# Optimization experiments

Hardware: AMD Instinct MI355X
Metric: run time of the kernel (lower is better)

Reference implementation:

```python
import jax, jax.numpy as jnp
import numpy as np

NUM_EXPERTS = 8
HIDDEN_DIM = 2048
EXPERT_DIM = 1408
TOP_K = 2
NUM_TOKENS = 8192


def setup_inputs() -> dict:
    key = jax.random.key(0)
    k_x, k_idx, k_s, k_up, k_dn = jax.random.split(key, 5)
    x = jax.random.normal(k_x, (NUM_TOKENS, HIDDEN_DIM), dtype=jnp.float32)
    expert_indices = jax.random.randint(k_idx, (NUM_TOKENS, TOP_K), 0, NUM_EXPERTS, dtype=jnp.int64)
    scores = jax.random.uniform(k_s, (NUM_TOKENS, TOP_K), dtype=jnp.float32)
    up_proj = jax.random.normal(k_up, (NUM_EXPERTS, HIDDEN_DIM, 2 * EXPERT_DIM), dtype=jnp.float32) * 0.02
    down_proj = jax.random.normal(k_dn, (NUM_EXPERTS, EXPERT_DIM, HIDDEN_DIM), dtype=jnp.float32) * 0.02
    return {"x": x, "expert_indices": expert_indices, "scores": scores,
            "up_proj": up_proj, "down_proj": down_proj}


def reference(x, expert_indices, scores, up_proj, down_proj):
    # x: [T, H]; expert_indices/scores: [T, K]; up_proj: [E, H, 2D]; down_proj: [E, D, H]
    E = up_proj.shape[0]
    D = down_proj.shape[1]
    out = jnp.zeros_like(x)
    # Loop over small fixed set of experts; each token's output is the score-weighted
    # sum over the experts it was routed to (SwiGLU gated FFN per expert).
    for e in range(E):
        # combined routing weight of expert e for each token: [T]
        w_e = jnp.sum(scores * (expert_indices == e).astype(scores.dtype), axis=-1)
        h = x @ up_proj[e]                      # [T, 2D]
        gate, up = h[:, :D], h[:, D:]
        y = (jax.nn.silu(gate) * up) @ down_proj[e]  # [T, H]
        out = out + w_e[:, None] * y
    return out
```

## Files before the change

### kernel.cpp

```cpp
#include <hip/hip_runtime.h>
#include <hip/hip_bf16.h>
#include <cstdint>
#include <cstddef>

#define N_EXPERTS 8
#define HIDDEN    2048
#define EDIM      1408
#define UPCOLS    2816
#define NTOK      8192
#define CAP       8192
#define MAXMT     136
#define NS_UP     22
#define NS_DN     16
#define GUP       6
#define GDN       8

typedef __bf16 bf16x8 __attribute__((ext_vector_type(8)));
typedef __bf16 bf16x4 __attribute__((ext_vector_type(4)));
typedef float  f32x4  __attribute__((ext_vector_type(4)));

#define EPOS_OFF  4096
#define TOK_OFF   (EPOS_OFF + (size_t)NTOK * 2 * 4)
#define W_OFF     (TOK_OFF + (size_t)CAP * N_EXPERTS * 4)
#define XBF_OFF   (W_OFF + (size_t)CAP * N_EXPERTS * 4)
#define UPT_OFF   (XBF_OFF + (size_t)NTOK * HIDDEN * 2)
#define DNT_OFF   (UPT_OFF + (size_t)N_EXPERTS * UPCOLS * HIDDEN * 2)
#define HACT_OFF  (DNT_OFF + (size_t)N_EXPERTS * HIDDEN * EDIM * 2)
#define WS_NEEDED (HACT_OFF + (size_t)(MAXMT * 128) * EDIM * 2)
#define YBUF_OFF  UPT_OFF


__device__ __forceinline__ void gload16(const void* g, void* l) {
  __builtin_amdgcn_global_load_lds(
      (const __attribute__((address_space(1))) void*)g,
      (__attribute__((address_space(3))) void*)l, 16, 0, 0);
}

__global__ void build_entries(const int* __restrict__ idx,
                              const float* __restrict__ sc,
                              int* __restrict__ meta,
                              int* __restrict__ toks,
                              float* __restrict__ wts,
                              int* __restrict__ epos) {
  int t = blockIdx.x * blockDim.x + threadIdx.x;
  if (t >= NTOK) return;
  int e0 = idx[2 * t] & 7, e1 = idx[2 * t + 1] & 7;
  float s0 = sc[2 * t], s1 = sc[2 * t + 1];
  if (e0 == e1) {
    int p = atomicAdd(&meta[e0], 1);
    toks[e0 * CAP + p] = t; wts[e0 * CAP + p] = s0 + s1;
    epos[2 * t] = (e0 << 16) | p; epos[2 * t + 1] = -1;
  } else {
    int p0 = atomicAdd(&meta[e0], 1);
    toks[e0 * CAP + p0] = t; wts[e0 * CAP + p0] = s0;
    int p1 = atomicAdd(&meta[e1], 1);
    toks[e1 * CAP + p1] = t; wts[e1 * CAP + p1] = s1;
    epos[2 * t] = (e0 << 16) | p0; epos[2 * t + 1] = (e1 << 16) | p1;
  }
}

__global__ void finalize_meta(int* __restrict__ meta,
                              int* __restrict__ toks,
                              float* __restrict__ wts) {
  __shared__ int c[8], pc[8];
  int tid = threadIdx.x;
  if (tid < 8) { c[tid] = meta[tid]; pc[tid] = ((c[tid] + 127) >> 7) << 7; }
  __syncthreads();
  if (tid == 0) {
    int off = 0, t = 0;
    for (int e = 0; e < 8; e++) {
      meta[16 + e] = off;
      int nt = pc[e] >> 7;
      for (int i = 0; i < nt; i++) { meta[32 + t] = e; meta[192 + t] = i * 128; t++; }
      off += pc[e];
    }
    meta[8] = t;
  }
  for (int e = 0; e < 8; e++)
    for (int i = c[e] + tid; i < pc[e]; i += blockDim.x) {
      toks[e * CAP + i] = 0; wts[e * CAP + i] = 0.f;
    }
}

__global__ void cast_x(const float4* __restrict__ in, __bf16* __restrict__ o) {
  size_t i = (size_t)blockIdx.x * blockDim.x + threadIdx.x;
  float4 v = in[i];
  bf16x4 r = { (__bf16)v.x, (__bf16)v.y, (__bf16)v.z, (__bf16)v.w };
  ((bf16x4*)o)[i] = r;
}

__global__ void transpose_cast(const float* __restrict__ in, __bf16* __restrict__ out,
                               int K, int N) {
  __shared__ float t[32][33];
  const size_t ebase = (size_t)blockIdx.z * K * N;
  const float* src = in + ebase;
  __bf16* dst = out + ebase;
  int x0 = blockIdx.x * 32, y0 = blockIdx.y * 32;
  int tx = threadIdx.x, ty = threadIdx.y;
#pragma unroll
  for (int i = 0; i < 4; i++)
    t[ty + 8 * i][tx] = src[(size_t)(y0 + ty + 8 * i) * N + x0 + tx];
  __syncthreads();
#pragma unroll
  for (int i = 0; i < 4; i++)
    dst[(size_t)(x0 + ty + 8 * i) * K + y0 + tx] = (__bf16)t[tx][ty + 8 * i];
}


__global__ __launch_bounds__(256, 4) void gemm_up(
    const __bf16* __restrict__ xb, const __bf16* __restrict__ upT,
    const int* __restrict__ meta, const int* __restrict__ toks,
    __bf16* __restrict__ hact) {
  const int rank = (blockIdx.x & 7) * (MAXMT * NS_UP / 8) + (blockIdx.x >> 3);
  const int vt = rank / NS_UP;
  if (vt >= meta[8]) return;
  const int e = meta[32 + vt];
  const int tb = vt - (meta[192 + vt] >> 7);
  const int tiles_e = (meta[e] + 127) >> 7;
  int rem = rank - NS_UP * tb;
  int g = 0, tleft = tiles_e;
  for (;;) {
    int gsz = tleft < GUP ? tleft : GUP;
    int span = NS_UP * gsz;
    if (rem < span) break;
    rem -= span; tleft -= GUP; g++;
  }
  const int gsz = tleft < GUP ? tleft : GUP;
  const int s = rem / gsz, tix = rem - s * gsz;
  const int row0 = (g * GUP + tix) * 128;
  const int hbase = meta[16 + e];
  const int n0 = s * 64;

  __shared__ __bf16 lA[128 * 64];
  __shared__ __bf16 lBg[64 * 64];
  __shared__ __bf16 lBu[64 * 64];

  const int tid = threadIdx.x;
  const int lane = tid & 63, wave = tid >> 6;
  const int srow = tid >> 3;
  const int gch = (tid & 7) ^ (srow & 7);

  const __bf16* upE = upT + (size_t)e * UPCOLS * HIDDEN;

  size_t aoff[4];
#pragma unroll
  for (int r = 0; r < 4; r++) {
    int row = row0 + srow + 32 * r;
    int tok = toks[e * CAP + row];
    aoff[r] = (size_t)tok * HIDDEN + gch * 8;
  }
  size_t bgoff[2], buoff[2];
#pragma unroll
  for (int r = 0; r < 2; r++) {
    int n = n0 + srow + 32 * r;
    bgoff[r] = (size_t)n * HIDDEN + gch * 8;
    buoff[r] = (size_t)(n + EDIM) * HIDDEN + gch * 8;
  }

  f32x4 accg[4][2] = {};
  f32x4 accu[4][2] = {};
  const int wrow = (wave >> 1) * 64;
  const int wcol = (wave & 1) * 32;
  const int l15 = lane & 15, quad = lane >> 4;

  for (int k0 = 0; k0 < HIDDEN; k0 += 64) {
    __syncthreads();
#pragma unroll
    for (int r = 0; r < 4; r++)
      gload16(xb + aoff[r] + k0, (char*)lA + r * 4096 + tid * 16);
#pragma unroll
    for (int r = 0; r < 2; r++) {
      gload16(upE + bgoff[r] + k0, (char*)lBg + r * 4096 + tid * 16);
      gload16(upE + buoff[r] + k0, (char*)lBu + r * 4096 + tid * 16);
    }
    __syncthreads();
#pragma unroll
    for (int kk = 0; kk < 2; kk++) {
      bf16x8 af[4], bg[2], bu[2];
#pragma unroll
      for (int mi = 0; mi < 4; mi++) {
        int row = wrow + mi * 16 + l15;
        int slot = (kk * 4 + quad) ^ (row & 7);
        af[mi] = *(const bf16x8*)((const char*)lA + row * 128 + slot * 16);
      }
#pragma unroll
      for (int ni = 0; ni < 2; ni++) {
        int row = wcol + ni * 16 + l15;
        int slot = (kk * 4 + quad) ^ (row & 7);
        bg[ni] = *(const bf16x8*)((const char*)lBg + row * 128 + slot * 16);
        bu[ni] = *(const bf16x8*)((const char*)lBu + row * 128 + slot * 16);
      }
#pragma unroll
      for (int mi = 0; mi < 4; mi++)
#pragma unroll
        for (int ni = 0; ni < 2; ni++) {
          accg[mi][ni] = __builtin_amdgcn_mfma_f32_16x16x32_bf16(af[mi], bg[ni], accg[mi][ni], 0, 0, 0);
          accu[mi][ni] = __builtin_amdgcn_mfma_f32_16x16x32_bf16(af[mi], bu[ni], accu[mi][ni], 0, 0, 0);
        }
    }
  }

#pragma unroll
  for (int mi = 0; mi < 4; mi++)
#pragma unroll
    for (int ni = 0; ni < 2; ni++)
#pragma unroll
      for (int v = 0; v < 4; v++) {
        int m = hbase + row0 + wrow + mi * 16 + quad * 4 + v;
        int n = n0 + wcol + ni * 16 + l15;
        float g = accg[mi][ni][v];
        float u = accu[mi][ni][v];
        float act = g / (1.f + __expf(-g)) * u;
        hact[(size_t)m * EDIM + n] = (__bf16)act;
      }
}

__global__ __launch_bounds__(256, 4) void gemm_down(
    const __bf16* __restrict__ hact, const __bf16* __restrict__ dnT,
    const int* __restrict__ meta, const float* __restrict__ wts,
    __bf16* __restrict__ ybuf) {
  const int rank = (blockIdx.x & 7) * (MAXMT * NS_DN / 8) + (blockIdx.x >> 3);
  const int vt = rank / NS_DN;
  if (vt >= meta[8]) return;
  const int e = meta[32 + vt];
  const int tb = vt - (meta[192 + vt] >> 7);
  const int tiles_e = (meta[e] + 127) >> 7;
  int rem = rank - NS_DN * tb;
  int g = 0, tleft = tiles_e;
  for (;;) {
    int gsz = tleft < GDN ? tleft : GDN;
    int span = NS_DN * gsz;
    if (rem < span) break;
    rem -= span; tleft -= GDN; g++;
  }
  const int gsz = tleft < GDN ? tleft : GDN;
  const int s = rem / gsz, tix = rem - s * gsz;
  const int row0 = (g * GDN + tix) * 128;
  const int hbase = meta[16 + e];
  const int n0 = s * 128;

  __shared__ __bf16 lA[128 * 64];
  __shared__ __bf16 lB[128 * 64];

  const int tid = threadIdx.x;
  const int lane = tid & 63, wave = tid >> 6;
  const int srow = tid >> 3;
  const int gch = (tid & 7) ^ (srow & 7);

  const __bf16* dnE = dnT + (size_t)e * HIDDEN * EDIM;

  size_t aoff[4], boff[4];
#pragma unroll
  for (int r = 0; r < 4; r++) {
    int row = srow + 32 * r;
    aoff[r] = (size_t)(hbase + row0 + row) * EDIM + gch * 8;
    boff[r] = (size_t)(n0 + row) * EDIM + gch * 8;
  }

  f32x4 acc[4][4] = {};
  const int wrow = (wave >> 1) * 64;
  const int wcol = (wave & 1) * 64;
  const int l15 = lane & 15, quad = lane >> 4;

  for (int k0 = 0; k0 < EDIM; k0 += 64) {
    __syncthreads();
#pragma unroll
    for (int r = 0; r < 4; r++) {
      gload16(hact + aoff[r] + k0, (char*)lA + r * 4096 + tid * 16);
      gload16(dnE + boff[r] + k0, (char*)lB + r * 4096 + tid * 16);
    }
    __syncthreads();
#pragma unroll
    for (int kk = 0; kk < 2; kk++) {
      bf16x8 af[4], bfr[4];
#pragma unroll
      for (int mi = 0; mi < 4; mi++) {
        int row = wrow + mi * 16 + l15;
        int slot = (kk * 4 + quad) ^ (row & 7);
        af[mi] = *(const bf16x8*)((const char*)lA + row * 128 + slot * 16);
      }
#pragma unroll
      for (int ni = 0; ni < 4; ni++) {
        int row = wcol + ni * 16 + l15;
        int slot = (kk * 4 + quad) ^ (row & 7);
        bfr[ni] = *(const bf16x8*)((const char*)lB + row * 128 + slot * 16);
      }
#pragma unroll
      for (int mi = 0; mi < 4; mi++)
#pragma unroll
        for (int ni = 0; ni < 4; ni++)
          acc[mi][ni] = __builtin_amdgcn_mfma_f32_16x16x32_bf16(af[mi], bfr[ni], acc[mi][ni], 0, 0, 0);
    }
  }

#pragma unroll
  for (int mi = 0; mi < 4; mi++)
#pragma unroll
    for (int v = 0; v < 4; v++) {
      int rloc = row0 + wrow + mi * 16 + quad * 4 + v;
      float w = wts[e * CAP + rloc];
      size_t g2 = (size_t)(hbase + rloc) * HIDDEN;
#pragma unroll
      for (int ni = 0; ni < 4; ni++) {
        int n = n0 + wcol + ni * 16 + l15;
        ybuf[g2 + n] = (__bf16)(acc[mi][ni][v] * w);
      }
    }
}

__global__ __launch_bounds__(256) void combine(
    const __bf16* __restrict__ ybuf, const int* __restrict__ epos,
    const int* __restrict__ meta, float* __restrict__ out) {
  const int t = blockIdx.x;
  const int c = threadIdx.x * 8;
  const int p0 = epos[2 * t], p1 = epos[2 * t + 1];
  const int e0 = p0 >> 16;
  const size_t g0 = (size_t)(meta[16 + e0] + (p0 & 0xffff)) * HIDDEN;
  bf16x8 y0 = *(const bf16x8*)(ybuf + g0 + c);
  float acc[8];
#pragma unroll
  for (int j = 0; j < 8; j++) acc[j] = (float)y0[j];
  if (p1 >= 0) {
    const int e1 = p1 >> 16;
    const size_t g1 = (size_t)(meta[16 + e1] + (p1 & 0xffff)) * HIDDEN;
    bf16x8 y1 = *(const bf16x8*)(ybuf + g1 + c);
#pragma unroll
    for (int j = 0; j < 8; j++) acc[j] += (float)y1[j];
  }
  float4* o = (float4*)(out + (size_t)t * HIDDEN + c);
  o[0] = make_float4(acc[0], acc[1], acc[2], acc[3]);
  o[1] = make_float4(acc[4], acc[5], acc[6], acc[7]);
}

extern "C" void kernel_launch(void* const* d_in, const int* in_sizes, int n_in,
                              void* d_out, int out_size, void* d_ws, size_t ws_size,
                              hipStream_t stream) {
  const float* x = (const float*)d_in[0];
  const int* idx = (const int*)d_in[1];
  const float* sc = (const float*)d_in[2];
  const float* up = (const float*)d_in[3];
  const float* dn = (const float*)d_in[4];
  float* out = (float*)d_out;
  char* ws = (char*)d_ws;

  if (ws_size < WS_NEEDED) return;

  int* meta = (int*)ws;
  int* epos = (int*)(ws + EPOS_OFF);
  int* toks = (int*)(ws + TOK_OFF);
  float* wts = (float*)(ws + W_OFF);
  __bf16* xb = (__bf16*)(ws + XBF_OFF);
  __bf16* upT = (__bf16*)(ws + UPT_OFF);
  __bf16* dnT = (__bf16*)(ws + DNT_OFF);
  __bf16* hact = (__bf16*)(ws + HACT_OFF);
  __bf16* ybuf = (__bf16*)(ws + YBUF_OFF);

  hipMemsetAsync(meta, 0, 64, stream);

  build_entries<<<NTOK / 256, 256, 0, stream>>>(idx, sc, meta, toks, wts, epos);
  finalize_meta<<<1, 256, 0, stream>>>(meta, toks, wts);
  cast_x<<<(NTOK * HIDDEN / 4) / 256, 256, 0, stream>>>((const float4*)x, xb);
  dim3 tb(32, 8);
  transpose_cast<<<dim3(UPCOLS / 32, HIDDEN / 32, N_EXPERTS), tb, 0, stream>>>(up, upT, HIDDEN, UPCOLS);
  transpose_cast<<<dim3(HIDDEN / 32, EDIM / 32, N_EXPERTS), tb, 0, stream>>>(dn, dnT, EDIM, HIDDEN);
  gemm_up<<<MAXMT * NS_UP, 256, 0, stream>>>(xb, upT, meta, toks, hact);
  gemm_down<<<MAXMT * NS_DN, 256, 0, stream>>>(hact, dnT, meta, wts, ybuf);
  combine<<<NTOK, 256, 0, stream>>>(ybuf, epos, meta, out);
}
```

Baseline: 766.3 us.

## Use 256x256 tiles with double-buffered LDS pipeline in expert GEMMs

Both expert GEMMs move from 128-row tiles on 256 threads to 256-row by 256-column tiles on 512 threads (8 waves), padding expert capacity to multiples of 256. LDS is double-buffered so the next K slice is loaded asynchronously while MFMAs run on the current one, and the MFMA sections use explicit barriers and setprio. The aim is more data reuse per tile, fewer global loads per flop, and hiding load latency. In exchange, padding waste grows, fewer blocks are launched with 128KB of LDS each, and one-block-per-CU occupancy risks idle CUs on a few tail tiles.

New measurement: 936.7 us. 1.22x slower.

```diff
diff --git a/kernel.cpp b/kernel.cpp
--- a/kernel.cpp
+++ b/kernel.cpp
@@ -9,11 +9,13 @@
 #define UPCOLS    2816
 #define NTOK      8192
 #define CAP       8192
-#define MAXMT     136
-#define NS_UP     22
-#define NS_DN     16
-#define GUP       6
-#define GDN       8
+#define MAXT      72
+#define NS_UP     11
+#define NS_DN     8
+#define GUP       3
+#define GDN       4
+#define NT_UP     32
+#define NT_DN     22
 
 typedef __bf16 bf16x8 __attribute__((ext_vector_type(8)));
 typedef __bf16 bf16x4 __attribute__((ext_vector_type(4)));
@@ -26,7 +28,8 @@
 #define UPT_OFF   (XBF_OFF + (size_t)NTOK * HIDDEN * 2)
 #define DNT_OFF   (UPT_OFF + (size_t)N_EXPERTS * UPCOLS * HIDDEN * 2)
 #define HACT_OFF  (DNT_OFF + (size_t)N_EXPERTS * HIDDEN * EDIM * 2)
-#define WS_NEEDED (HACT_OFF + (size_t)(MAXMT * 128) * EDIM * 2)
+#define HACT_ROWS ((size_t)MAXT * 256)
+#define WS_NEEDED (HACT_OFF + HACT_ROWS * EDIM * 2)
 #define YBUF_OFF  UPT_OFF
 
 
@@ -64,14 +67,14 @@
                               float* __restrict__ wts) {
   __shared__ int c[8], pc[8];
   int tid = threadIdx.x;
-  if (tid < 8) { c[tid] = meta[tid]; pc[tid] = ((c[tid] + 127) >> 7) << 7; }
+  if (tid < 8) { c[tid] = meta[tid]; pc[tid] = ((c[tid] + 255) >> 8) << 8; }
   __syncthreads();
   if (tid == 0) {
     int off = 0, t = 0;
     for (int e = 0; e < 8; e++) {
       meta[16 + e] = off;
-      int nt = pc[e] >> 7;
-      for (int i = 0; i < nt; i++) { meta[32 + t] = e; meta[192 + t] = i * 128; t++; }
+      int nt = pc[e] >> 8;
+      for (int i = 0; i < nt; i++) { meta[32 + t] = e; meta[192 + t] = i * 256; t++; }
       off += pc[e];
     }
     meta[8] = t;
@@ -107,16 +110,16 @@
 }
 
 
-__global__ __launch_bounds__(256, 4) void gemm_up(
+__global__ __launch_bounds__(512, 2) void gemm_up(
     const __bf16* __restrict__ xb, const __bf16* __restrict__ upT,
     const int* __restrict__ meta, const int* __restrict__ toks,
     __bf16* __restrict__ hact) {
-  const int rank = (blockIdx.x & 7) * (MAXMT * NS_UP / 8) + (blockIdx.x >> 3);
+  const int rank = (blockIdx.x & 7) * (MAXT * NS_UP / 8) + (blockIdx.x >> 3);
   const int vt = rank / NS_UP;
   if (vt >= meta[8]) return;
   const int e = meta[32 + vt];
-  const int tb = vt - (meta[192 + vt] >> 7);
-  const int tiles_e = (meta[e] + 127) >> 7;
+  const int tb = vt - (meta[192 + vt] >> 8);
+  const int tiles_e = (meta[e] + 255) >> 8;
   int rem = rank - NS_UP * tb;
   int g = 0, tleft = tiles_e;
   for (;;) {
@@ -127,104 +130,128 @@
   }
   const int gsz = tleft < GUP ? tleft : GUP;
   const int s = rem / gsz, tix = rem - s * gsz;
-  const int row0 = (g * GUP + tix) * 128;
+  const int row0 = (g * GUP + tix) * 256;
   const int hbase = meta[16 + e];
-  const int n0 = s * 64;
-
-  __shared__ __bf16 lA[128 * 64];
-  __shared__ __bf16 lBg[64 * 64];
-  __shared__ __bf16 lBu[64 * 64];
+  const int n0 = s * 128;
+
+  __shared__ __attribute__((aligned(16))) char lds[131072];
 
   const int tid = threadIdx.x;
   const int lane = tid & 63, wave = tid >> 6;
+  const int wm = wave >> 2, wn = wave & 3;
+  const int l15 = lane & 15, quad = lane >> 4;
   const int srow = tid >> 3;
   const int gch = (tid & 7) ^ (srow & 7);
 
   const __bf16* upE = upT + (size_t)e * UPCOLS * HIDDEN;
 
-  size_t aoff[4];
+  size_t aoff[4], boff[4];
 #pragma unroll
   for (int r = 0; r < 4; r++) {
-    int row = row0 + srow + 32 * r;
+    int row = row0 + r * 64 + srow;
     int tok = toks[e * CAP + row];
     aoff[r] = (size_t)tok * HIDDEN + gch * 8;
   }
-  size_t bgoff[2], buoff[2];
-#pragma unroll
-  for (int r = 0; r < 2; r++) {
-    int n = n0 + srow + 32 * r;
-    bgoff[r] = (size_t)n * HIDDEN + gch * 8;
-    buoff[r] = (size_t)(n + EDIM) * HIDDEN + gch * 8;
-  }
-
-  f32x4 accg[4][2] = {};
-  f32x4 accu[4][2] = {};
-  const int wrow = (wave >> 1) * 64;
-  const int wcol = (wave & 1) * 32;
-  const int l15 = lane & 15, quad = lane >> 4;
-
-  for (int k0 = 0; k0 < HIDDEN; k0 += 64) {
-    __syncthreads();
-#pragma unroll
-    for (int r = 0; r < 4; r++)
-      gload16(xb + aoff[r] + k0, (char*)lA + r * 4096 + tid * 16);
-#pragma unroll
-    for (int r = 0; r < 2; r++) {
-      gload16(upE + bgoff[r] + k0, (char*)lBg + r * 4096 + tid * 16);
-      gload16(upE + buoff[r] + k0, (char*)lBu + r * 4096 + tid * 16);
+#pragma unroll
+  for (int j = 0; j < 4; j++) {
+    int grow = (srow < 32) ? (n0 + 32 * j + srow)
+                           : (EDIM + n0 + 32 * j + (srow - 32));
+    boff[j] = (size_t)grow * HIDDEN + gch * 8;
+  }
+
+  f32x4 acc[2][2][4][2] = {};
+
+  const int sl0 = (quad ^ (l15 & 7)) * 16;
+  const int sl1 = ((4 + quad) ^ (l15 & 7)) * 16;
+  const int aRowBase = wm * 16384 + l15 * 128;
+  const int bRowBase = 65536 + (wn >> 1) * 16384 + ((wn & 1) * 64 + l15) * 128;
+
+#define STAGE_UP(buf, k0) do {                                          \
+    char* _a = lds + (buf) * 32768;                                     \
+    char* _bb = lds + 65536 + (buf) * 32768;                            \
+    _Pragma("unroll")                                                   \
+    for (int r = 0; r < 4; r++)                                         \
+      gload16(xb + aoff[r] + (k0), _a + r * 8192 + tid * 16);           \
+    _Pragma("unroll")                                                   \
+    for (int r = 0; r < 4; r++)                                         \
+      gload16(upE + boff[r] + (k0), _bb + r * 8192 + tid * 16);         \
+  } while (0)
+
+#define PHASE_UP(cbuf, rh, ch) do {                                     \
+    const char* _l = lds + (cbuf) * 32768;                              \
+    bf16x8 a0[4], a1[4], b0[2], b1[2];                                  \
+    _Pragma("unroll")                                                   \
+    for (int mi = 0; mi < 4; mi++) {                                    \
+      int rb = aRowBase + (rh) * 8192 + mi * 2048;                      \
+      a0[mi] = *(const bf16x8*)(_l + rb + sl0);                         \
+      a1[mi] = *(const bf16x8*)(_l + rb + sl1);                         \
+    }                                                                   \
+    _Pragma("unroll")                                                   \
+    for (int ni = 0; ni < 2; ni++) {                                    \
+      int rb = bRowBase + (ch) * 4096 + ni * 2048;                      \
+      b0[ni] = *(const bf16x8*)(_l + rb + sl0);                         \
+      b1[ni] = *(const bf16x8*)(_l + rb + sl1);                         \
+    }                                                                   \
+    __builtin_amdgcn_s_barrier();                                       \
+    __builtin_amdgcn_s_setprio(1);                                      \
+    _Pragma("unroll")                                                   \
+    for (int mi = 0; mi < 4; mi++)                                      \
+      _Pragma("unroll")                                                 \
+      for (int ni = 0; ni < 2; ni++) {                                  \
+        acc[rh][ch][mi][ni] = __builtin_amdgcn_mfma_f32_16x16x32_bf16(  \
+            a0[mi], b0[ni], acc[rh][ch][mi][ni], 0, 0, 0);              \
+        acc[rh][ch][mi][ni] = __builtin_amdgcn_mfma_f32_16x16x32_bf16(  \
+            a1[mi], b1[ni], acc[rh][ch][mi][ni], 0, 0, 0);              \
+      }                                                                 \
+    __builtin_amdgcn_s_setprio(0);                                      \
+    __builtin_amdgcn_s_barrier();                                       \
+  } while (0)
+
+  STAGE_UP(0, 0);
+#pragma unroll 1
+  for (int kt = 0; kt < NT_UP; ++kt) {
+    const int c = kt & 1;
+    if (kt + 1 < NT_UP) {
+      STAGE_UP(c ^ 1, (kt + 1) * 64);
+      asm volatile("s_waitcnt vmcnt(8)" ::: "memory");
+    } else {
+      asm volatile("s_waitcnt vmcnt(0)" ::: "memory");
     }
-    __syncthreads();
-#pragma unroll
-    for (int kk = 0; kk < 2; kk++) {
-      bf16x8 af[4], bg[2], bu[2];
-#pragma unroll
-      for (int mi = 0; mi < 4; mi++) {
-        int row = wrow + mi * 16 + l15;
-        int slot = (kk * 4 + quad) ^ (row & 7);
-        af[mi] = *(const bf16x8*)((const char*)lA + row * 128 + slot * 16);
+    __builtin_amdgcn_s_barrier();
+    PHASE_UP(c, 0, 0); PHASE_UP(c, 0, 1);
+    PHASE_UP(c, 1, 0); PHASE_UP(c, 1, 1);
+  }
+#undef STAGE_UP
+#undef PHASE_UP
+
+#pragma unroll
+  for (int rh = 0; rh < 2; rh++)
+#pragma unroll
+    for (int mi = 0; mi < 4; mi++)
+#pragma unroll
+      for (int v = 0; v < 4; v++) {
+        int m = hbase + row0 + wm * 128 + rh * 64 + mi * 16 + quad * 4 + v;
+#pragma unroll
+        for (int ni = 0; ni < 2; ni++) {
+          int n = n0 + wn * 32 + ni * 16 + l15;
+          float gg = acc[rh][0][mi][ni][v];
+          float uu = acc[rh][1][mi][ni][v];
+          float act = gg / (1.f + __expf(-gg)) * uu;
+          hact[(size_t)m * EDIM + n] = (__bf16)act;
+        }
       }
-#pragma unroll
-      for (int ni = 0; ni < 2; ni++) {
-        int row = wcol + ni * 16 + l15;
-        int slot = (kk * 4 + quad) ^ (row & 7);
-        bg[ni] = *(const bf16x8*)((const char*)lBg + row * 128 + slot * 16);
-        bu[ni] = *(const bf16x8*)((const char*)lBu + row * 128 + slot * 16);
-      }
-#pragma unroll
-      for (int mi = 0; mi < 4; mi++)
-#pragma unroll
-        for (int ni = 0; ni < 2; ni++) {
-          accg[mi][ni] = __builtin_amdgcn_mfma_f32_16x16x32_bf16(af[mi], bg[ni], accg[mi][ni], 0, 0, 0);
-          accu[mi][ni] = __builtin_amdgcn_mfma_f32_16x16x32_bf16(af[mi], bu[ni], accu[mi][ni], 0, 0, 0);
-        }
-    }
-  }
-
-#pragma unroll
-  for (int mi = 0; mi < 4; mi++)
-#pragma unroll
-    for (int ni = 0; ni < 2; ni++)
-#pragma unroll
-      for (int v = 0; v < 4; v++) {
-        int m = hbase + row0 + wrow + mi * 16 + quad * 4 + v;
-        int n = n0 + wcol + ni * 16 + l15;
-        float g = accg[mi][ni][v];
-        float u = accu[mi][ni][v];
-        float act = g / (1.f + __expf(-g)) * u;
-        hact[(size_t)m * EDIM + n] = (__bf16)act;
-      }
-}
-
-__global__ __launch_bounds__(256, 4) void gemm_down(
+}
+
+__global__ __launch_bounds__(512, 2) void gemm_down(
     const __bf16* __restrict__ hact, const __bf16* __restrict__ dnT,
     const int* __restrict__ meta, const float* __restrict__ wts,
     __bf16* __restrict__ ybuf) {
-  const int rank = (blockIdx.x & 7) * (MAXMT * NS_DN / 8) + (blockIdx.x >> 3);
+  const int rank = (blockIdx.x & 7) * (MAXT * NS_DN / 8) + (blockIdx.x >> 3);
   const int vt = rank / NS_DN;
   if (vt >= meta[8]) return;
   const int e = meta[32 + vt];
-  const int tb = vt - (meta[192 + vt] >> 7);
-  const int tiles_e = (meta[e] + 127) >> 7;
+  const int tb = vt - (meta[192 + vt] >> 8);
+  const int tiles_e = (meta[e] + 255) >> 8;
   int rem = rank - NS_DN * tb;
   int g = 0, tleft = tiles_e;
   for (;;) {
@@ -235,15 +262,16 @@
   }
   const int gsz = tleft < GDN ? tleft : GDN;
   const int s = rem / gsz, tix = rem - s * gsz;
-  const int row0 = (g * GDN + tix) * 128;
+  const int row0 = (g * GDN + tix) * 256;
   const int hbase = meta[16 + e];
-  const int n0 = s * 128;
-
-  __shared__ __bf16 lA[128 * 64];
-  __shared__ __bf16 lB[128 * 64];
+  const int n0 = s * 256;
+
+  __shared__ __attribute__((aligned(16))) char lds[131072];
 
   const int tid = threadIdx.x;
   const int lane = tid & 63, wave = tid >> 6;
+  const int wm = wave >> 2, wn = wave & 3;
+  const int l15 = lane & 15, quad = lane >> 4;
   const int srow = tid >> 3;
   const int gch = (tid & 7) ^ (srow & 7);
 
@@ -252,60 +280,93 @@
   size_t aoff[4], boff[4];
 #pragma unroll
   for (int r = 0; r < 4; r++) {
-    int row = srow + 32 * r;
-    aoff[r] = (size_t)(hbase + row0 + row) * EDIM + gch * 8;
-    boff[r] = (size_t)(n0 + row) * EDIM + gch * 8;
-  }
-
-  f32x4 acc[4][4] = {};
-  const int wrow = (wave >> 1) * 64;
-  const int wcol = (wave & 1) * 64;
-  const int l15 = lane & 15, quad = lane >> 4;
-
-  for (int k0 = 0; k0 < EDIM; k0 += 64) {
-    __syncthreads();
-#pragma unroll
-    for (int r = 0; r < 4; r++) {
-      gload16(hact + aoff[r] + k0, (char*)lA + r * 4096 + tid * 16);
-      gload16(dnE + boff[r] + k0, (char*)lB + r * 4096 + tid * 16);
+    aoff[r] = (size_t)(hbase + row0 + r * 64 + srow) * EDIM + gch * 8;
+    boff[r] = (size_t)(n0 + r * 64 + srow) * EDIM + gch * 8;
+  }
+
+  f32x4 acc[2][2][4][2] = {};
+
+  const int sl0 = (quad ^ (l15 & 7)) * 16;
+  const int sl1 = ((4 + quad) ^ (l15 & 7)) * 16;
+  const int aRowBase = wm * 16384 + l15 * 128;
+  const int bRowBase = 65536 + (wn >> 1) * 16384 + ((wn & 1) * 64 + l15) * 128;
+
+#define STAGE_DN(buf, k0) do {                                          \
+    char* _a = lds + (buf) * 32768;                                     \
+    char* _bb = lds + 65536 + (buf) * 32768;                            \
+    _Pragma("unroll")                                                   \
+    for (int r = 0; r < 4; r++)                                         \
+      gload16(hact + aoff[r] + (k0), _a + r * 8192 + tid * 16);         \
+    _Pragma("unroll")                                                   \
+    for (int r = 0; r < 4; r++)                                         \
+      gload16(dnE + boff[r] + (k0), _bb + r * 8192 + tid * 16);         \
+  } while (0)
+
+#define PHASE_DN(cbuf, rh, ch) do {                                     \
+    const char* _l = lds + (cbuf) * 32768;                              \
+    bf16x8 a0[4], a1[4], b0[2], b1[2];                                  \
+    _Pragma("unroll")                                                   \
+    for (int mi = 0; mi < 4; mi++) {                                    \
+      int rb = aRowBase + (rh) * 8192 + mi * 2048;                      \
+      a0[mi] = *(const bf16x8*)(_l + rb + sl0);                         \
+      a1[mi] = *(const bf16x8*)(_l + rb + sl1);                         \
+    }                                                                   \
+    _Pragma("unroll")                                                   \
+    for (int ni = 0; ni < 2; ni++) {                                    \
+      int rb = bRowBase + (ch) * 4096 + ni * 2048;                      \
+      b0[ni] = *(const bf16x8*)(_l + rb + sl0);                         \
+      b1[ni] = *(const bf16x8*)(_l + rb + sl1);                         \
+    }                                                                   \
+    __builtin_amdgcn_s_barrier();                                       \
+    __builtin_amdgcn_s_setprio(1);                                      \
+    _Pragma("unroll")                                                   \
+    for (int mi = 0; mi < 4; mi++)                                      \
+      _Pragma("unroll")                                                 \
+      for (int ni = 0; ni < 2; ni++) {                                  \
+        acc[rh][ch][mi][ni] = __builtin_amdgcn_mfma_f32_16x16x32_bf16(  \
+            a0[mi], b0[ni], acc[rh][ch][mi][ni], 0, 0, 0);              \
+        acc[rh][ch][mi][ni] = __builtin_amdgcn_mfma_f32_16x16x32_bf16(  \
+            a1[mi], b1[ni], acc[rh][ch][mi][ni], 0, 0, 0);              \
+      }                                                                 \
+    __builtin_amdgcn_s_setprio(0);                                      \
+    __builtin_amdgcn_s_barrier();                                       \
+  } while (0)
+
+  STAGE_DN(0, 0);
+#pragma unroll 1
+  for (int kt = 0; kt < NT_DN; ++kt) {
+    const int c = kt & 1;
+    if (kt + 1 < NT_DN) {
+      STAGE_DN(c ^ 1, (kt + 1) * 64);
+      asm volatile("s_waitcnt vmcnt(8)" ::: "memory");
+    } else {
+      asm volatile("s_waitcnt vmcnt(0)" ::: "memory");
     }
-    __syncthreads();
-#pragma unroll
-    for (int kk = 0; kk < 2; kk++) {
-      bf16x8 af[4], bfr[4];
-#pragma unroll
-      for (int mi = 0; mi < 4; mi++) {
-        int row = wrow + mi * 16 + l15;
-        int slot = (kk * 4 + quad) ^ (row & 7);
-        af[mi] = *(const bf16x8*)((const char*)lA + row * 128 + slot * 16);
+    __builtin_amdgcn_s_barrier();
+    PHASE_DN(c, 0, 0); PHASE_DN(c, 0, 1);
+    PHASE_DN(c, 1, 0); PHASE_DN(c, 1, 1);
+  }
+#undef STAGE_DN
+#undef PHASE_DN
+
+#pragma unroll
+  for (int rh = 0; rh < 2; rh++)
+#pragma unroll
+    for (int mi = 0; mi < 4; mi++)
+#pragma unroll
+      for (int v = 0; v < 4; v++) {
+        int rloc = row0 + wm * 128 + rh * 64 + mi * 16 + quad * 4 + v;
+        float w = wts[e * CAP + rloc];
+        size_t gb = (size_t)(hbase + rloc) * HIDDEN;
+#pragma unroll
+        for (int ni = 0; ni < 2; ni++) {
+#pragma unroll
+          for (int ch = 0; ch < 2; ch++) {
+            int n = n0 + wn * 64 + ch * 32 + ni * 16 + l15;
+            ybuf[gb + n] = (__bf16)(acc[rh][ch][mi][ni][v] * w);
+          }
+        }
       }
-#pragma unroll
-      for (int ni = 0; ni < 4; ni++) {
-        int row = wcol + ni * 16 + l15;
-        int slot = (kk * 4 + quad) ^ (row & 7);
-        bfr[ni] = *(const bf16x8*)((const char*)lB + row * 128 + slot * 16);
-      }
-#pragma unroll
-      for (int mi = 0; mi < 4; mi++)
-#pragma unroll
-        for (int ni = 0; ni < 4; ni++)
-          acc[mi][ni] = __builtin_amdgcn_mfma_f32_16x16x32_bf16(af[mi], bfr[ni], acc[mi][ni], 0, 0, 0);
-    }
-  }
-
-#pragma unroll
-  for (int mi = 0; mi < 4; mi++)
-#pragma unroll
-    for (int v = 0; v < 4; v++) {
-      int rloc = row0 + wrow + mi * 16 + quad * 4 + v;
-      float w = wts[e * CAP + rloc];
-      size_t g2 = (size_t)(hbase + rloc) * HIDDEN;
-#pragma unroll
-      for (int ni = 0; ni < 4; ni++) {
-        int n = n0 + wcol + ni * 16 + l15;
-        ybuf[g2 + n] = (__bf16)(acc[mi][ni][v] * w);
-      }
-    }
 }
 
 __global__ __launch_bounds__(256) void combine(
@@ -363,7 +424,7 @@
   dim3 tb(32, 8);
   transpose_cast<<<dim3(UPCOLS / 32, HIDDEN / 32, N_EXPERTS), tb, 0, stream>>>(up, upT, HIDDEN, UPCOLS);
   transpose_cast<<<dim3(HIDDEN / 32, EDIM / 32, N_EXPERTS), tb, 0, stream>>>(dn, dnT, EDIM, HIDDEN);
-  gemm_up<<<MAXMT * NS_UP, 256, 0, stream>>>(xb, upT, meta, toks, hact);
-  gemm_down<<<MAXMT * NS_DN, 256, 0, stream>>>(hact, dnT, meta, wts, ybuf);
+  gemm_up<<<MAXT * NS_UP, 512, 0, stream>>>(xb, upT, meta, toks, hact);
+  gemm_down<<<MAXT * NS_DN, 512, 0, stream>>>(hact, dnT, meta, wts, ybuf);
   combine<<<NTOK, 256, 0, stream>>>(ybuf, epos, meta, out);
 }
```
